# Kernel optimization log

Measured on AMD Instinct MI355X. Metric: run time of the kernel, lower is better.

Reference implementation:

```python
import jax, jax.numpy as jnp
import numpy as np

B, H, W, C = 8, 64, 64, 512
C8, C2 = C // 8, C // 2  # f/g channels = 64, h channels = 256 (divisor = 2)


def _maxpool2x2(t):
    # [B, H, W, F] -> [B, H//2, W//2, F], valid 2x2 max pooling
    b, h, w, f = t.shape
    return t.reshape(b, h // 2, 2, w // 2, 2, f).max(axis=(2, 4))


def setup_inputs() -> dict:
    key = jax.random.key(0)
    kx, kf, kg, kh, ko, kgam = jax.random.split(key, 6)
    sf = lambda fan_in: (1.0 / np.sqrt(fan_in)).astype(np.float32)
    return {
        "x": jax.random.normal(kx, (B, H, W, C), dtype=jnp.float32),
        "wf": jax.random.normal(kf, (C, C8), dtype=jnp.float32) * sf(C),
        "wg": jax.random.normal(kg, (C, C8), dtype=jnp.float32) * sf(C),
        "wh": jax.random.normal(kh, (C, C2), dtype=jnp.float32) * sf(C),
        "wo": jax.random.normal(ko, (C2, C), dtype=jnp.float32) * sf(C2),
        "gamma": jax.random.normal(kgam, (1,), dtype=jnp.float32) * 0.1,
    }


def reference(x, wf, wg, wh, wo, gamma):
    b = x.shape[0]
    # 1x1 convs == channel matmuls
    f = _maxpool2x2(jnp.einsum("bhwc,cd->bhwd", x, wf)).reshape(b, -1, C8)  # [B, N/4, C/8]
    g = jnp.einsum("bhwc,cd->bhwd", x, wg).reshape(b, -1, C8)               # [B, N,   C/8]
    s = jnp.einsum("bqd,bkd->bqk", g, f)                                     # unscaled scores
    beta = jax.nn.softmax(s, axis=-1)
    h = _maxpool2x2(jnp.einsum("bhwc,cd->bhwd", x, wh)).reshape(b, -1, C2)  # [B, N/4, C/2]
    o = jnp.einsum("bqk,bkd->bqd", beta, h).reshape(b, H, W, C2)
    o = jnp.einsum("bhwd,dc->bhwc", o, wo)                                   # o_conv back to C
    return gamma * o + x
```

## Files before the change

### kernel.cpp

```cpp
#include <hip/hip_runtime.h>
#include <hip/hip_bf16.h>

#define NTOK 4096
#define NPOOL 1024

using short8 = __attribute__((ext_vector_type(8))) short;
using f32x4  = __attribute__((ext_vector_type(4))) float;

__device__ __forceinline__ unsigned short f2bf(float f) {
  __hip_bfloat16 h = __float2bfloat16(f);
  return __builtin_bit_cast(unsigned short, h);
}

__device__ __forceinline__ int pool_row(int bx, int m) {
  int pg = bx * 16 + (m >> 2);
  int corner = m & 3;
  int batch = pg >> 10;
  int pl = pg & 1023;
  int pi = pl >> 5, pj = pl & 31;
  return (batch << 12) + ((2 * pi + (corner >> 1)) << 6) + 2 * pj + (corner & 1);
}

__global__ __launch_bounds__(256) void pack_w(const float* __restrict__ wf,
                                              const float* __restrict__ wg,
                                              const float* __restrict__ wh,
                                              const float* __restrict__ wo,
                                              unsigned short* __restrict__ wcatT,
                                              unsigned short* __restrict__ woT) {
  int i = blockIdx.x * 256 + threadIdx.x;
  if (i < 384 * 512) {
    int n = i >> 9, k = i & 511;
    float v = (n < 64) ? wf[k * 64 + n]
            : (n < 128) ? wg[k * 64 + (n - 64)]
                        : wh[k * 256 + (n - 128)];
    wcatT[i] = f2bf(v);
  } else if (i < 384 * 512 + 512 * 256) {
    int j = i - 384 * 512;
    int n = j >> 8, k = j & 255;
    woT[j] = f2bf(wo[(size_t)k * 512 + n]);
  }
}

__global__ __launch_bounds__(512) void fgh_proj(const float* __restrict__ x,
                                                const unsigned short* __restrict__ wcatT,
                                                unsigned short* __restrict__ fB,
                                                unsigned short* __restrict__ gB,
                                                unsigned short* __restrict__ hT) {
  __shared__ unsigned short lds[33280];
  const int tid = threadIdx.x;
  const int bx = blockIdx.x;
  const int wave = tid >> 6, lane = tid & 63;
  const int col = lane & 15, rgrp = lane >> 4;
  const int wcol = wave * 48;

  {
    const int xm = tid >> 3, xk4 = (tid & 7) << 2;
    const float* xrow = x + (size_t)pool_row(bx, xm) * 512 + xk4;
    unsigned short* dst = &lds[xm * 520 + xk4];
#pragma unroll
    for (int kt = 0; kt < 16; ++kt) {
      float4 v = *(const float4*)(xrow + kt * 32);
      ushort4 o4;
      o4.x = f2bf(v.x); o4.y = f2bf(v.y); o4.z = f2bf(v.z); o4.w = f2bf(v.w);
      *(ushort4*)(dst + kt * 32) = o4;
    }
  }
  __syncthreads();

  f32x4 acc[4][3];
#pragma unroll
  for (int mt = 0; mt < 4; ++mt)
#pragma unroll
    for (int nt = 0; nt < 3; ++nt) acc[mt][nt] = (f32x4){0.f, 0.f, 0.f, 0.f};

  for (int kt = 0; kt < 16; ++kt) {
    short8 am[4];
#pragma unroll
    for (int mt = 0; mt < 4; ++mt)
      am[mt] = *(const short8*)&lds[(mt * 16 + col) * 520 + kt * 32 + rgrp * 8];
#pragma unroll
    for (int nt = 0; nt < 3; ++nt) {
      short8 bn = *(const short8*)(wcatT + (size_t)(wcol + nt * 16 + col) * 512 + kt * 32 + rgrp * 8);
#pragma unroll
      for (int mt = 0; mt < 4; ++mt)
        acc[mt][nt] = __builtin_amdgcn_mfma_f32_16x16x32_bf16(am[mt], bn, acc[mt][nt], 0, 0, 0);
    }
  }
  __syncthreads();

  unsigned short* gO = lds;
  unsigned short* fO = lds + 4608;
  unsigned short* hO = lds + 5760;
#pragma unroll
  for (int mt = 0; mt < 4; ++mt) {
#pragma unroll
    for (int nt = 0; nt < 3; ++nt) {
      int n = wcol + nt * 16 + col;
      f32x4 a = acc[mt][nt];
      if (n < 64) {
        float mx = fmaxf(fmaxf(a[0], a[1]), fmaxf(a[2], a[3]));
        fO[(mt * 4 + rgrp) * 72 + n] = f2bf(mx);
      } else if (n < 128) {
#pragma unroll
        for (int reg = 0; reg < 4; ++reg)
          gO[(mt * 16 + rgrp * 4 + reg) * 72 + (n - 64)] = f2bf(a[reg]);
      } else {
        float mx = fmaxf(fmaxf(a[0], a[1]), fmaxf(a[2], a[3]));
        hO[(n - 128) * 24 + (mt * 4 + rgrp)] = f2bf(mx);
      }
    }
  }
  __syncthreads();

  const int b = bx >> 6, pkb = (bx & 63) * 16;
  {
    int m = tid >> 3, d8 = (tid & 7) << 3;
    *(uint4*)(gB + (size_t)pool_row(bx, m) * 64 + d8) = *(const uint4*)&gO[m * 72 + d8];
  }
  if (tid < 128) {
    int pr = tid >> 3, d8 = (tid & 7) << 3;
    *(uint4*)(fB + (size_t)(bx * 16 + pr) * 64 + d8) = *(const uint4*)&fO[pr * 72 + d8];
  }
  {
    int dv = tid >> 1, p8 = (tid & 1) << 3;
    *(uint4*)(hT + (((size_t)b * 256 + dv) << 10) + pkb + p8) = *(const uint4*)&hO[dv * 24 + p8];
  }
}

__global__ __launch_bounds__(512) void attn_mfma(const __hip_bfloat16* __restrict__ G,
                                                 const __hip_bfloat16* __restrict__ F,
                                                 const __hip_bfloat16* __restrict__ HT,
                                                 unsigned short* __restrict__ O) {
  __shared__ unsigned short lds[33792];

  const int tid = threadIdx.x;
  const int wave = tid >> 6, lane = tid & 63;
  const int col = lane & 15;
  const int rgrp = lane >> 4;
  const int b = blockIdx.x >> 5, qt = blockIdx.x & 31;

  const unsigned short* Gb = (const unsigned short*)G + ((size_t)b * NTOK + qt * 128) * 64;
  const unsigned short* Fb = (const unsigned short*)F + (size_t)b * NPOOL * 64;
  const unsigned short* Hb = (const unsigned short*)HT + (size_t)b * 256 * NPOOL;

  short8 ag[2];
#pragma unroll
  for (int ks = 0; ks < 2; ++ks)
    ag[ks] = *(const short8*)(Gb + (size_t)(wave * 16 + col) * 64 + ks * 32 + rgrp * 8);

  f32x4 oacc[16];
#pragma unroll
  for (int t = 0; t < 16; ++t) oacc[t] = (f32x4){0.f, 0.f, 0.f, 0.f};
  float m_run[4], l_run[4];
#pragma unroll
  for (int r = 0; r < 4; ++r) { m_run[r] = -1e30f; l_run[r] = 0.f; }

  const int fk = tid >> 3, fd8 = (tid & 7) << 3;

  for (int kc = 0; kc < 16; ++kc) {
    __syncthreads();
    *(uint4*)&lds[fk * 72 + fd8] =
        *(const uint4*)(Fb + (size_t)(kc * 64 + fk) * 64 + fd8);
#pragma unroll
    for (int r = 0; r < 4; ++r) {
      int j = tid + r * 512;
      int dv = j >> 3, k8 = (j & 7) << 3;
      *(uint4*)&lds[4608 + dv * 72 + k8] =
          *(const uint4*)(Hb + (size_t)dv * NPOOL + kc * 64 + k8);
    }
    __syncthreads();

    f32x4 s[4];
#pragma unroll
    for (int t = 0; t < 4; ++t) s[t] = (f32x4){0.f, 0.f, 0.f, 0.f};
#pragma unroll
    for (int ks = 0; ks < 2; ++ks) {
#pragma unroll
      for (int t = 0; t < 4; ++t) {
        short8 bf = *(const short8*)&lds[(t * 16 + col) * 72 + ks * 32 + rgrp * 8];
        s[t] = __builtin_amdgcn_mfma_f32_16x16x32_bf16(ag[ks], bf, s[t], 0, 0, 0);
      }
    }

    float cm[4];
#pragma unroll
    for (int r = 0; r < 4; ++r) {
      cm[r] = fmaxf(fmaxf(s[0][r], s[1][r]), fmaxf(s[2][r], s[3][r]));
#pragma unroll
      for (int msk = 1; msk < 16; msk <<= 1) cm[r] = fmaxf(cm[r], __shfl_xor(cm[r], msk));
    }
    bool upd = false;
#pragma unroll
    for (int r = 0; r < 4; ++r) upd |= (cm[r] > m_run[r]);
    if (__any(upd)) {
      float alpha[4];
#pragma unroll
      for (int r = 0; r < 4; ++r) {
        float mn = fmaxf(m_run[r], cm[r]);
        alpha[r] = __expf(m_run[r] - mn);
        m_run[r] = mn;
        l_run[r] *= alpha[r];
      }
#pragma unroll
      for (int t = 0; t < 16; ++t) {
#pragma unroll
        for (int r = 0; r < 4; ++r) oacc[t][r] *= alpha[r];
      }
    }

    float rs[4] = {0.f, 0.f, 0.f, 0.f};
    const int prow = wave * 16 + rgrp * 4;
#pragma unroll
    for (int t = 0; t < 4; ++t) {
#pragma unroll
      for (int r = 0; r < 4; ++r) {
        float p = __expf(s[t][r] - m_run[r]);
        rs[r] += p;
        lds[23040 + (prow + r) * 72 + t * 16 + col] = f2bf(p);
      }
    }
#pragma unroll
    for (int r = 0; r < 4; ++r) {
#pragma unroll
      for (int msk = 1; msk < 16; msk <<= 1) rs[r] += __shfl_xor(rs[r], msk);
      l_run[r] += rs[r];
    }

    short8 ap[2];
#pragma unroll
    for (int ks = 0; ks < 2; ++ks)
      ap[ks] = *(const short8*)&lds[23040 + (wave * 16 + col) * 72 + ks * 32 + rgrp * 8];
#pragma unroll
    for (int t = 0; t < 16; ++t) {
#pragma unroll
      for (int ks = 0; ks < 2; ++ks) {
        short8 bh = *(const short8*)&lds[4608 + (t * 16 + col) * 72 + ks * 32 + rgrp * 8];
        oacc[t] = __builtin_amdgcn_mfma_f32_16x16x32_bf16(ap[ks], bh, oacc[t], 0, 0, 0);
      }
    }
  }

  float inv[4];
#pragma unroll
  for (int r = 0; r < 4; ++r) inv[r] = 1.0f / l_run[r];
  __syncthreads();
  const int qrow = wave * 16 + rgrp * 4;
#pragma unroll
  for (int t = 0; t < 16; ++t) {
#pragma unroll
    for (int r = 0; r < 4; ++r)
      lds[(qrow + r) * 264 + t * 16 + col] = f2bf(oacc[t][r] * inv[r]);
  }
  __syncthreads();
  unsigned short* Ob = O + ((size_t)b * NTOK + qt * 128) * 256;
#pragma unroll
  for (int r = 0; r < 8; ++r) {
    int idx = tid + r * 512;
    int q = idx >> 5, d8 = (idx & 31) << 3;
    *(uint4*)(Ob + (size_t)q * 256 + d8) = *(const uint4*)&lds[q * 264 + d8];
  }
}

__global__ __launch_bounds__(512) void gemm_out_mfma(const unsigned short* __restrict__ Obf,
                                                     const unsigned short* __restrict__ woT,
                                                     const float* __restrict__ Xres,
                                                     const float* __restrict__ gamma,
                                                     float* __restrict__ Out) {
  __shared__ unsigned short lds[16896];
  const int tid = threadIdx.x;
  const int bx = blockIdx.x;
  const int wave = tid >> 6, lane = tid & 63;
  const int col = lane & 15, rgrp = lane >> 4;
  const int wc = wave * 64;

#pragma unroll
  for (int r = 0; r < 4; ++r) {
    int idx = tid + r * 512;
    int m = idx >> 5, k8 = (idx & 31) << 3;
    *(uint4*)&lds[m * 264 + k8] =
        *(const uint4*)(Obf + ((size_t)bx * 64 + m) * 256 + k8);
  }
  __syncthreads();

  f32x4 acc[4][4];
#pragma unroll
  for (int mt = 0; mt < 4; ++mt)
#pragma unroll
    for (int nt = 0; nt < 4; ++nt) acc[mt][nt] = (f32x4){0.f, 0.f, 0.f, 0.f};

  for (int kt = 0; kt < 8; ++kt) {
    short8 am[4];
#pragma unroll
    for (int mt = 0; mt < 4; ++mt)
      am[mt] = *(const short8*)&lds[(mt * 16 + col) * 264 + kt * 32 + rgrp * 8];
#pragma unroll
    for (int nt = 0; nt < 4; ++nt) {
      short8 bn = *(const short8*)(woT + (size_t)(wc + nt * 16 + col) * 256 + kt * 32 + rgrp * 8);
#pragma unroll
      for (int mt = 0; mt < 4; ++mt)
        acc[mt][nt] = __builtin_amdgcn_mfma_f32_16x16x32_bf16(am[mt], bn, acc[mt][nt], 0, 0, 0);
    }
  }

  float gm = gamma[0];
#pragma unroll
  for (int mt = 0; mt < 4; ++mt) {
#pragma unroll
    for (int nt = 0; nt < 4; ++nt) {
      int n = wc + nt * 16 + col;
#pragma unroll
      for (int reg = 0; reg < 4; ++reg) {
        size_t row = (size_t)bx * 64 + mt * 16 + rgrp * 4 + reg;
        size_t off = row * 512 + n;
        Out[off] = gm * acc[mt][nt][reg] + Xres[off];
      }
    }
  }
}

extern "C" void kernel_launch(void* const* d_in, const int* in_sizes, int n_in,
                              void* d_out, int out_size, void* d_ws, size_t ws_size,
                              hipStream_t stream) {
  (void)in_sizes; (void)n_in; (void)out_size; (void)ws_size;
  const float* x     = (const float*)d_in[0];
  const float* wf    = (const float*)d_in[1];
  const float* wg    = (const float*)d_in[2];
  const float* wh    = (const float*)d_in[3];
  const float* wo    = (const float*)d_in[4];
  const float* gamma = (const float*)d_in[5];
  float* out = (float*)d_out;

  unsigned short* ws = (unsigned short*)d_ws;
  unsigned short* oB    = ws;
  unsigned short* gB    = ws + 8388608;
  unsigned short* fB    = ws + 10485760;
  unsigned short* hT    = ws + 11010048;
  unsigned short* wcatT = ws + 13107200;
  unsigned short* woT   = ws + 13303808;

  pack_w<<<1280, dim3(256), 0, stream>>>(wf, wg, wh, wo, wcatT, woT);
  fgh_proj<<<512, dim3(512), 0, stream>>>(x, wcatT, fB, gB, hT);
  attn_mfma<<<256, dim3(512), 0, stream>>>((const __hip_bfloat16*)gB, (const __hip_bfloat16*)fB,
                                           (const __hip_bfloat16*)hT, oB);
  gemm_out_mfma<<<512, dim3(512), 0, stream>>>(oB, woT, x, gamma, out);
}
```

Baseline: 229.2 us.

## Fuse output projection and residual into attention kernel epilogue

Removes the separate gemm_out kernel and the bf16 intermediate O buffer. The attention kernel now multiplies its normalized output tile in LDS by woT directly and writes gamma*o + x. This avoids a kernel launch and the global write and read of the 8x4096x256 intermediate. In exchange the output GEMM runs on only 256 blocks, each wave loading woT straight from global memory, which adds register pressure and a longer tail on the attention kernel.

```diff
diff --git a/kernel.cpp b/kernel.cpp
--- a/kernel.cpp
+++ b/kernel.cpp
@@ -130,7 +130,10 @@
 __global__ __launch_bounds__(512) void attn_mfma(const __hip_bfloat16* __restrict__ G,
                                                  const __hip_bfloat16* __restrict__ F,
                                                  const __hip_bfloat16* __restrict__ HT,
-                                                 unsigned short* __restrict__ O) {
+                                                 const unsigned short* __restrict__ woT,
+                                                 const float* __restrict__ Xres,
+                                                 const float* __restrict__ gamma,
+                                                 float* __restrict__ Out) {
   __shared__ unsigned short lds[33792];
 
   const int tid = threadIdx.x;
@@ -252,67 +255,30 @@
       lds[(qrow + r) * 264 + t * 16 + col] = f2bf(oacc[t][r] * inv[r]);
   }
   __syncthreads();
-  unsigned short* Ob = O + ((size_t)b * NTOK + qt * 128) * 256;
-#pragma unroll
-  for (int r = 0; r < 8; ++r) {
-    int idx = tid + r * 512;
-    int q = idx >> 5, d8 = (idx & 31) << 3;
-    *(uint4*)(Ob + (size_t)q * 256 + d8) = *(const uint4*)&lds[q * 264 + d8];
-  }
-}
-
-__global__ __launch_bounds__(512) void gemm_out_mfma(const unsigned short* __restrict__ Obf,
-                                                     const unsigned short* __restrict__ woT,
-                                                     const float* __restrict__ Xres,
-                                                     const float* __restrict__ gamma,
-                                                     float* __restrict__ Out) {
-  __shared__ unsigned short lds[16896];
-  const int tid = threadIdx.x;
-  const int bx = blockIdx.x;
-  const int wave = tid >> 6, lane = tid & 63;
-  const int col = lane & 15, rgrp = lane >> 4;
-  const int wc = wave * 64;
-
-#pragma unroll
-  for (int r = 0; r < 4; ++r) {
-    int idx = tid + r * 512;
-    int m = idx >> 5, k8 = (idx & 31) << 3;
-    *(uint4*)&lds[m * 264 + k8] =
-        *(const uint4*)(Obf + ((size_t)bx * 64 + m) * 256 + k8);
-  }
-  __syncthreads();
-
-  f32x4 acc[4][4];
-#pragma unroll
-  for (int mt = 0; mt < 4; ++mt)
-#pragma unroll
-    for (int nt = 0; nt < 4; ++nt) acc[mt][nt] = (f32x4){0.f, 0.f, 0.f, 0.f};
-
-  for (int kt = 0; kt < 8; ++kt) {
-    short8 am[4];
-#pragma unroll
-    for (int mt = 0; mt < 4; ++mt)
-      am[mt] = *(const short8*)&lds[(mt * 16 + col) * 264 + kt * 32 + rgrp * 8];
-#pragma unroll
-    for (int nt = 0; nt < 4; ++nt) {
-      short8 bn = *(const short8*)(woT + (size_t)(wc + nt * 16 + col) * 256 + kt * 32 + rgrp * 8);
-#pragma unroll
-      for (int mt = 0; mt < 4; ++mt)
-        acc[mt][nt] = __builtin_amdgcn_mfma_f32_16x16x32_bf16(am[mt], bn, acc[mt][nt], 0, 0, 0);
-    }
-  }
-
-  float gm = gamma[0];
-#pragma unroll
-  for (int mt = 0; mt < 4; ++mt) {
-#pragma unroll
-    for (int nt = 0; nt < 4; ++nt) {
-      int n = wc + nt * 16 + col;
+
+  const float gm = gamma[0];
+  const size_t rowbase = (size_t)b * NTOK + (size_t)qt * 128 + wave * 16;
+#pragma unroll
+  for (int c = 0; c < 4; ++c) {
+    f32x4 acc2[8];
+#pragma unroll
+    for (int nt = 0; nt < 8; ++nt) acc2[nt] = (f32x4){0.f, 0.f, 0.f, 0.f};
+#pragma unroll
+    for (int kt = 0; kt < 8; ++kt) {
+      short8 am = *(const short8*)&lds[(wave * 16 + col) * 264 + kt * 32 + rgrp * 8];
+#pragma unroll
+      for (int nt = 0; nt < 8; ++nt) {
+        short8 bn = *(const short8*)(woT + (size_t)(c * 128 + nt * 16 + col) * 256 + kt * 32 + rgrp * 8);
+        acc2[nt] = __builtin_amdgcn_mfma_f32_16x16x32_bf16(am, bn, acc2[nt], 0, 0, 0);
+      }
+    }
+#pragma unroll
+    for (int nt = 0; nt < 8; ++nt) {
+      int n = c * 128 + nt * 16 + col;
 #pragma unroll
       for (int reg = 0; reg < 4; ++reg) {
-        size_t row = (size_t)bx * 64 + mt * 16 + rgrp * 4 + reg;
-        size_t off = row * 512 + n;
-        Out[off] = gm * acc[mt][nt][reg] + Xres[off];
+        size_t off = (rowbase + rgrp * 4 + reg) * 512 + n;
+        Out[off] = gm * acc2[nt][reg] + Xres[off];
       }
     }
   }
@@ -331,7 +297,6 @@
   float* out = (float*)d_out;
 
   unsigned short* ws = (unsigned short*)d_ws;
-  unsigned short* oB    = ws;
   unsigned short* gB    = ws + 8388608;
   unsigned short* fB    = ws + 10485760;
   unsigned short* hT    = ws + 11010048;
@@ -341,6 +306,5 @@
   pack_w<<<1280, dim3(256), 0, stream>>>(wf, wg, wh, wo, wcatT, woT);
   fgh_proj<<<512, dim3(512), 0, stream>>>(x, wcatT, fB, gB, hT);
   attn_mfma<<<256, dim3(512), 0, stream>>>((const __hip_bfloat16*)gB, (const __hip_bfloat16*)fB,
-                                           (const __hip_bfloat16*)hT, oB);
-  gemm_out_mfma<<<512, dim3(512), 0, stream>>>(oB, woT, x, gamma, out);
-}
+                                           (const __hip_bfloat16*)hT, woT, x, gamma, out);
+}
```

Result: slower. 287.3 us (+25.3%).
